# Kernel tuning notes

Measured on AMD Instinct MI355X. Metric: run time of the kernel, lower is better.

Reference implementation:

```python
import jax, jax.numpy as jnp
import numpy as np

TOPK = 20
N_SAMPLES = 100  # selects_each_sample in the torch code
SQRT2 = 1.4142   # constant used by the torch code


def _normalize(pts):
    # pts: [B,N,3] homogeneous points; weights are all-ones in the torch call path.
    c = pts.mean(axis=1)                                   # [B,3]
    d = pts - c[:, None, :]
    meandist = jnp.sqrt(d[..., 0] ** 2 + d[..., 1] ** 2).mean(axis=1)  # [B]
    s = SQRT2 / meandist
    z = jnp.zeros_like(s)
    o = jnp.ones_like(s)
    T = jnp.stack([
        jnp.stack([s, z, -c[:, 0] * s], axis=-1),
        jnp.stack([z, s, -c[:, 1] * s], axis=-1),
        jnp.stack([z, z, o], axis=-1),
    ], axis=1)                                             # [B,3,3]
    ptsn = jnp.einsum('bij,bnj->bin', T, pts)              # [B,3,N]
    return ptsn, T


def _weighted_svd(pts1, pts2, weights):
    # pts*: [B,N,3], weights: [B,1,N]. Batched (vectorized) version of the
    # per-sample torch.svd loop: smallest right-singular vector of X via eigh
    # of the 9x9 Gram matrix, then rank-2 projection of the 3x3 F via SVD.
    w = weights[:, 0, :, None]                             # [B,N,1]
    p1n, T1 = _normalize(pts1)
    p2n, T2 = _normalize(pts2)
    p = jnp.concatenate([p2n[:, 0:1] * p1n, p2n[:, 1:2] * p1n, p1n], axis=1)  # [B,9,N]
    p = jnp.swapaxes(p, 1, 2)                              # [B,N,9]
    p = p / jnp.linalg.norm(p, axis=2, keepdims=True)      # normalize_SVD=True
    X = p * w                                              # [B,N,9]
    G = jnp.einsum('bni,bnj->bij', X, X)                   # [B,9,9]
    _, evecs = jnp.linalg.eigh(G)
    v = evecs[..., 0]                                      # [B,9] min-eigvec == V[:,-1] of svd(X)
    # canonical sign (torch SVD sign is arbitrary): largest-|.| entry positive
    imax = jnp.argmax(jnp.abs(v), axis=1)
    sgn = jnp.sign(jnp.take_along_axis(v, imax[:, None], axis=1))
    v = v * sgn                                            # unit norm already
    Fm = v.reshape(-1, 3, 3)
    U, S, Vh = jnp.linalg.svd(Fm, full_matrices=False)
    S2 = S * jnp.array([1.0, 1.0, 0.0], dtype=S.dtype)     # mask = [1,1,0]
    F_ = (U * S2[:, None, :]) @ Vh                         # rank-2 projection
    out = jnp.einsum('bji,bjk,bkl->bil', T2, F_, T1)       # T2^T @ F_ @ T1
    residual = jnp.einsum('bni,bi->bn', X, v)              # [B,N]
    return out, residual


def _forward(pts1, pts2, weights, unique_nums, sampled_idx):
    B, N, _ = pts1.shape
    # 1) full weighted 8-point fit
    out, residual = _weighted_svd(pts1, pts2, weights)
    wvec = weights[:, 0, :]                                # [B,N]
    # 2) topK fit over the first `unique_num` entries (masked top_k)
    valid = jnp.arange(N)[None, :] < unique_nums[:, None]
    wm = jnp.where(valid, wvec, -jnp.inf)
    _, idx = jax.lax.top_k(wm, TOPK)                       # [B,20]
    pts1_k = jnp.take_along_axis(pts1, idx[:, :, None], axis=1)
    pts2_k = jnp.take_along_axis(pts2, idx[:, :, None], axis=1)
    w_k = jnp.take_along_axis(wvec, idx, axis=1)[:, None, :]  # [B,1,20]
    out_k, res_k = _weighted_svd(pts1_k, pts2_k, w_k)
    # 3) weighted random subsets (indices precomputed in setup_inputs)
    S_, K_ = sampled_idx.shape[1], sampled_idx.shape[2]
    bidx = jnp.arange(B)[:, None, None]
    p1s = pts1[bidx, sampled_idx]                          # [B,S,K,3]
    p2s = pts2[bidx, sampled_idx]
    ws = wvec[bidx, sampled_idx]                           # [B,S,K]
    w_accu = jnp.prod(ws * 1000.0, axis=2)                 # [B,S]
    w_accu = w_accu / (w_accu.sum(axis=1, keepdims=True) + 1e-10)
    out_s, _ = _weighted_svd(p1s.reshape(B * S_, K_, 3),
                             p2s.reshape(B * S_, K_, 3),
                             ws.reshape(B * S_, 1, K_))
    out_s = out_s.reshape(B, S_, 3, 3)
    return (out, residual, out_k, res_k, out_s, w_accu[..., None])


def setup_inputs() -> dict:
    B, N = 128, 8192
    key = jax.random.key(0)
    k1, k2, k3, k4 = jax.random.split(key, 4)
    pts1 = jax.random.normal(k1, (B, N, 3), dtype=jnp.float32).at[..., 2].set(1.0)
    pts2 = jax.random.normal(k2, (B, N, 3), dtype=jnp.float32).at[..., 2].set(1.0)
    # small positive weights so prod(w*1000, K=20) stays in fp32 range
    weights = jax.random.uniform(k3, (B, 1, N), dtype=jnp.float32) * 0.01 + 1e-6
    un = jax.random.randint(k4, (B,), 1024, N + 1).astype(jnp.int32)
    # per-sample weighted sampling (np.random.choice in the torch code)
    wnp = np.asarray(weights)[:, 0, :].astype(np.float64)
    un_np = np.asarray(un)
    rng = np.random.default_rng(0)
    sampled = np.empty((B, N_SAMPLES, TOPK), np.int32)
    for b in range(B):
        m = int(un_np[b])
        p = wnp[b, :m] / wnp[b, :m].sum()
        sampled[b] = rng.choice(m, size=(N_SAMPLES, TOPK), p=p).astype(np.int32)
    return {"pts1": pts1, "pts2": pts2, "weights": weights,
            "matches_good_unique_nums": un, "sampled_idx": jnp.asarray(sampled)}


def reference(pts1, pts2, weights, matches_good_unique_nums, sampled_idx):
    # returns (out, residual, out_topK, residual_topK,
    #          out_sample_selected_batch, weights_sample_selected_accu_batch)
    return _forward(pts1, pts2, weights, matches_good_unique_nums, sampled_idx)
```

## Files before the change

kernel.cpp:

```cpp
#include <hip/hip_runtime.h>
#include <math.h>

#define NPTS   8192
#define NB     128
#define TOPKN  20
#define NSAMP  100
#define NPROB  (NB + NB + NB * NSAMP)
#define SQRT2C 1.4142

#define OFF_OUT  0
#define OFF_RES  1152
#define OFF_OUTK 1049728
#define OFF_RESK 1050880
#define OFF_OUTS 1053440
#define OFF_WACC 1168640

#define WS_G    0
#define WS_TP   4700160
#define WS_V    5326848
#define WS_TOPK 6266880

__device__ __forceinline__ constexpr int tri9(int i, int j) {
  int a = i < j ? i : j;
  int b = i < j ? j : i;
  return a * 9 - a * (a - 1) / 2 + (b - a);
}

__global__ __launch_bounds__(1024) void prep_kernel(
    const float* __restrict__ pts1, const float* __restrict__ pts2,
    const float* __restrict__ wv, const int* __restrict__ un,
    int* __restrict__ topkidx, double* __restrict__ Gall,
    double* __restrict__ Tpall) {
  __shared__ float sw[NPTS];
  __shared__ float r16a[16], r16b[16], r16c[16], r16d[16];
  __shared__ int   i16[16];
  __shared__ double sred[16][45];
  __shared__ float sbc[6];
  const int tid = threadIdx.x, lane = tid & 63, wid = tid >> 6;

  if (blockIdx.x < NB) {
    const int b = blockIdx.x;
    const int m = un[b];
    const int mlim = (m + 1023) & ~1023;
    for (int n = tid; n < mlim; n += 1024)
      sw[n] = (n < m) ? wv[(size_t)b * NPTS + n] : -INFINITY;
    __syncthreads();
    for (int k = 0; k < TOPKN; ++k) {
      float best = -INFINITY; int bi = 0x7fffffff;
      for (int n = tid; n < mlim; n += 1024) {
        float v = sw[n];
        if (v > best) { best = v; bi = n; }
      }
      #pragma unroll
      for (int off = 32; off > 0; off >>= 1) {
        float ov = __shfl_down(best, off);
        int   oi = __shfl_down(bi, off);
        if (ov > best || (ov == best && oi < bi)) { best = ov; bi = oi; }
      }
      if (lane == 0) { r16a[wid] = best; i16[wid] = bi; }
      __syncthreads();
      if (wid == 0) {
        float v = (lane < 16) ? r16a[lane] : -INFINITY;
        int  ix = (lane < 16) ? i16[lane] : 0x7fffffff;
        #pragma unroll
        for (int off = 8; off > 0; off >>= 1) {
          float ov = __shfl_down(v, off);
          int   oi = __shfl_down(ix, off);
          if (ov > v || (ov == v && oi < ix)) { v = ov; ix = oi; }
        }
        if (lane == 0) { topkidx[b * TOPKN + k] = ix; sw[ix] = -INFINITY; }
      }
      __syncthreads();
    }
    return;
  }

  const int b = blockIdx.x - NB;
  const float* P1 = pts1 + (size_t)b * NPTS * 3;
  const float* P2 = pts2 + (size_t)b * NPTS * 3;
  const float* W  = wv   + (size_t)b * NPTS;

  float x1[8], y1[8], x2[8], y2[8], ww8[8];
  #pragma unroll
  for (int i = 0; i < 8; ++i) {
    const int n = tid + i * 1024;
    x1[i] = P1[n * 3]; y1[i] = P1[n * 3 + 1];
    x2[i] = P2[n * 3]; y2[i] = P2[n * 3 + 1];
    ww8[i] = W[n];
  }

  float sx1 = 0, sy1 = 0, sx2 = 0, sy2 = 0;
  #pragma unroll
  for (int i = 0; i < 8; ++i) { sx1 += x1[i]; sy1 += y1[i]; sx2 += x2[i]; sy2 += y2[i]; }
  #pragma unroll
  for (int off = 32; off > 0; off >>= 1) {
    sx1 += __shfl_down(sx1, off); sy1 += __shfl_down(sy1, off);
    sx2 += __shfl_down(sx2, off); sy2 += __shfl_down(sy2, off);
  }
  if (lane == 0) { r16a[wid] = sx1; r16b[wid] = sy1; r16c[wid] = sx2; r16d[wid] = sy2; }
  __syncthreads();
  if (wid == 0) {
    float a = (lane < 16) ? r16a[lane] : 0.f;
    float bb = (lane < 16) ? r16b[lane] : 0.f;
    float c = (lane < 16) ? r16c[lane] : 0.f;
    float d = (lane < 16) ? r16d[lane] : 0.f;
    #pragma unroll
    for (int off = 8; off > 0; off >>= 1) {
      a += __shfl_down(a, off); bb += __shfl_down(bb, off);
      c += __shfl_down(c, off); d += __shfl_down(d, off);
    }
    if (lane == 0) {
      sbc[0] = a / NPTS; sbc[1] = bb / NPTS; sbc[2] = c / NPTS; sbc[3] = d / NPTS;
    }
  }
  __syncthreads();
  const float cx1 = sbc[0], cy1 = sbc[1], cx2 = sbc[2], cy2 = sbc[3];

  float d1 = 0, d2 = 0;
  #pragma unroll
  for (int i = 0; i < 8; ++i) {
    float ax = x1[i] - cx1, ay = y1[i] - cy1;
    float bx = x2[i] - cx2, by = y2[i] - cy2;
    d1 += sqrtf(ax * ax + ay * ay);
    d2 += sqrtf(bx * bx + by * by);
  }
  #pragma unroll
  for (int off = 32; off > 0; off >>= 1) { d1 += __shfl_down(d1, off); d2 += __shfl_down(d2, off); }
  __syncthreads();
  if (lane == 0) { r16a[wid] = d1; r16b[wid] = d2; }
  __syncthreads();
  if (wid == 0) {
    float a = (lane < 16) ? r16a[lane] : 0.f;
    float bb = (lane < 16) ? r16b[lane] : 0.f;
    #pragma unroll
    for (int off = 8; off > 0; off >>= 1) { a += __shfl_down(a, off); bb += __shfl_down(bb, off); }
    if (lane == 0) {
      sbc[4] = (float)SQRT2C / (a / NPTS);
      sbc[5] = (float)SQRT2C / (bb / NPTS);
    }
  }
  __syncthreads();
  const float s1 = sbc[4], s2 = sbc[5];

  float g[45];
  #pragma unroll
  for (int i = 0; i < 45; ++i) g[i] = 0.f;
  #pragma unroll
  for (int i = 0; i < 8; ++i) {
    float p1x = s1 * (x1[i] - cx1), p1y = s1 * (y1[i] - cy1);
    float p2x = s2 * (x2[i] - cx2), p2y = s2 * (y2[i] - cy2);
    float f[9] = { p2x * p1x, p2x * p1y, p2x,
                   p2y * p1x, p2y * p1y, p2y,
                   p1x, p1y, 1.f };
    float n2 = 0.f;
    #pragma unroll
    for (int j = 0; j < 9; ++j) n2 += f[j] * f[j];
    float sc = ww8[i] / sqrtf(n2);
    #pragma unroll
    for (int j = 0; j < 9; ++j) f[j] *= sc;
    int t = 0;
    #pragma unroll
    for (int a = 0; a < 9; ++a)
      #pragma unroll
      for (int c = a; c < 9; ++c) { g[t] += f[a] * f[c]; ++t; }
  }
  #pragma unroll
  for (int t = 0; t < 45; ++t) {
    float v = g[t];
    #pragma unroll
    for (int off = 32; off > 0; off >>= 1) v += __shfl_down(v, off);
    if (lane == 0) sred[wid][t] = (double)v;
  }
  __syncthreads();
  if (tid < 45) {
    double a = 0;
    #pragma unroll
    for (int w = 0; w < 16; ++w) a += sred[w][tid];
    Gall[(size_t)tid * NPROB + b] = a;
  }
  if (tid == 0) {
    Tpall[0 * NPROB + b] = (double)s1;  Tpall[1 * NPROB + b] = (double)cx1;
    Tpall[2 * NPROB + b] = (double)cy1; Tpall[3 * NPROB + b] = (double)s2;
    Tpall[4 * NPROB + b] = (double)cx2; Tpall[5 * NPROB + b] = (double)cy2;
  }
}

__global__ __launch_bounds__(256) void small_g_kernel(
    const float* __restrict__ pts1, const float* __restrict__ pts2,
    const float* __restrict__ wv, const int* __restrict__ topkidx,
    const int* __restrict__ sampled, double* __restrict__ Gall,
    double* __restrict__ Tpall) {
  const int p = blockIdx.x * blockDim.x + threadIdx.x;
  if (p >= NB + NB * NSAMP) return;
  const int prob = NB + p;
  int b; const int* idx;
  if (p < NB) { b = p; idx = topkidx + p * TOPKN; }
  else { int q = p - NB; b = q / NSAMP; idx = sampled + (size_t)q * TOPKN; }
  const float* P1 = pts1 + (size_t)b * NPTS * 3;
  const float* P2 = pts2 + (size_t)b * NPTS * 3;
  const float* W  = wv   + (size_t)b * NPTS;

  float x1[TOPKN], y1[TOPKN], x2[TOPKN], y2[TOPKN], ww[TOPKN];
  #pragma unroll
  for (int k = 0; k < TOPKN; ++k) {
    int n = idx[k];
    x1[k] = P1[n * 3]; y1[k] = P1[n * 3 + 1];
    x2[k] = P2[n * 3]; y2[k] = P2[n * 3 + 1];
    ww[k] = W[n];
  }
  float cx1 = 0, cy1 = 0, cx2 = 0, cy2 = 0;
  #pragma unroll
  for (int k = 0; k < TOPKN; ++k) { cx1 += x1[k]; cy1 += y1[k]; cx2 += x2[k]; cy2 += y2[k]; }
  cx1 /= TOPKN; cy1 /= TOPKN; cx2 /= TOPKN; cy2 /= TOPKN;
  float d1 = 0, d2 = 0;
  #pragma unroll
  for (int k = 0; k < TOPKN; ++k) {
    float ax = x1[k] - cx1, ay = y1[k] - cy1; d1 += sqrtf(ax * ax + ay * ay);
    float bx = x2[k] - cx2, by = y2[k] - cy2; d2 += sqrtf(bx * bx + by * by);
  }
  const float s1 = (float)SQRT2C / (d1 / TOPKN), s2 = (float)SQRT2C / (d2 / TOPKN);

  float g[45];
  #pragma unroll
  for (int i = 0; i < 45; ++i) g[i] = 0.f;
  #pragma unroll
  for (int k = 0; k < TOPKN; ++k) {
    float p1x = s1 * (x1[k] - cx1), p1y = s1 * (y1[k] - cy1);
    float p2x = s2 * (x2[k] - cx2), p2y = s2 * (y2[k] - cy2);
    float f[9] = { p2x * p1x, p2x * p1y, p2x,
                   p2y * p1x, p2y * p1y, p2y,
                   p1x, p1y, 1.f };
    float n2 = 0.f;
    #pragma unroll
    for (int i = 0; i < 9; ++i) n2 += f[i] * f[i];
    float sc = ww[k] / sqrtf(n2);
    #pragma unroll
    for (int i = 0; i < 9; ++i) f[i] *= sc;
    int t = 0;
    #pragma unroll
    for (int i = 0; i < 9; ++i)
      #pragma unroll
      for (int j = i; j < 9; ++j) { g[t] += f[i] * f[j]; ++t; }
  }
  #pragma unroll
  for (int i = 0; i < 45; ++i) Gall[(size_t)i * NPROB + prob] = (double)g[i];
  Tpall[0 * NPROB + prob] = (double)s1;  Tpall[1 * NPROB + prob] = (double)cx1;
  Tpall[2 * NPROB + prob] = (double)cy1; Tpall[3 * NPROB + prob] = (double)s2;
  Tpall[4 * NPROB + prob] = (double)cx2; Tpall[5 * NPROB + prob] = (double)cy2;
}

__global__ __launch_bounds__(64, 1) void solve_kernel(
    const double* __restrict__ Gall, const double* __restrict__ Tpall,
    double* __restrict__ vall, float* __restrict__ dout) {
  const int prob = blockIdx.x * 64 + threadIdx.x;
  if (prob >= NPROB) return;

  float g[45];
  #pragma unroll
  for (int i = 0; i < 45; ++i) g[i] = (float)Gall[(size_t)i * NPROB + prob];

  float Vf[9][9];
  #pragma unroll
  for (int i = 0; i < 9; ++i)
    #pragma unroll
    for (int j = 0; j < 9; ++j) Vf[i][j] = (i == j) ? 1.0f : 0.0f;

  for (int sweep = 0; sweep < 5; ++sweep) {
    #pragma unroll
    for (int p = 0; p < 9; ++p) {
      #pragma unroll
      for (int q = p + 1; q < 9; ++q) {
        float apq = g[tri9(p, q)];
        if (fabsf(apq) > 1e-30f) {
          float app = g[tri9(p, p)], aqq = g[tri9(q, q)];
          float thf = (aqq - app) / (2.0f * apq);
          float tf = 1.0f / (fabsf(thf) + sqrtf(1.0f + thf * thf));
          if (thf < 0.0f) tf = -tf;
          float cf = 1.0f / sqrtf(1.0f + tf * tf);
          float sf = tf * cf;
          float tauf = sf / (1.0f + cf);
          g[tri9(p, p)] = app - tf * apq;
          g[tri9(q, q)] = aqq + tf * apq;
          g[tri9(p, q)] = 0.0f;
          #pragma unroll
          for (int k = 0; k < 9; ++k) {
            if (k != p && k != q) {
              float akp = g[tri9(k, p)], akq = g[tri9(k, q)];
              g[tri9(k, p)] = akp - sf * (akq + tauf * akp);
              g[tri9(k, q)] = akq + sf * (akp - tauf * akq);
            }
          }
          #pragma unroll
          for (int k = 0; k < 9; ++k) {
            float a = Vf[k][p], b2 = Vf[k][q];
            Vf[k][p] = cf * a - sf * b2;
            Vf[k][q] = sf * a + cf * b2;
          }
        }
      }
    }
  }

  int imin = 0; float emin = g[tri9(0, 0)];
  #pragma unroll
  for (int i = 1; i < 9; ++i) {
    float d = g[tri9(i, i)];
    if (d < emin) { emin = d; imin = i; }
  }
  double v[9];
  #pragma unroll
  for (int k = 0; k < 9; ++k) v[k] = (double)Vf[k][0];
  #pragma unroll
  for (int j = 1; j < 9; ++j) {
    bool take = (j == imin);
    #pragma unroll
    for (int k = 0; k < 9; ++k) v[k] = take ? (double)Vf[k][j] : v[k];
  }
  {
    double n2 = 0;
    #pragma unroll
    for (int i = 0; i < 9; ++i) n2 += v[i] * v[i];
    double inv = 1.0 / sqrt(n2);
    #pragma unroll
    for (int i = 0; i < 9; ++i) v[i] *= inv;
  }
  int imax = 0; double amax = fabs(v[0]);
  #pragma unroll
  for (int i = 1; i < 9; ++i) { double a = fabs(v[i]); if (a > amax) { amax = a; imax = i; } }
  double vmax = v[0];
  #pragma unroll
  for (int i = 1; i < 9; ++i) vmax = (i == imax) ? v[i] : vmax;
  double sgn = (vmax > 0.0) ? 1.0 : ((vmax < 0.0) ? -1.0 : 0.0);
  #pragma unroll
  for (int i = 0; i < 9; ++i) v[i] *= sgn;

  #pragma unroll
  for (int i = 0; i < 9; ++i) vall[(size_t)i * NPROB + prob] = v[i];

  double F[3][3] = { { v[0], v[1], v[2] }, { v[3], v[4], v[5] }, { v[6], v[7], v[8] } };
  double M[3][3];
  #pragma unroll
  for (int i = 0; i < 3; ++i)
    #pragma unroll
    for (int j = 0; j < 3; ++j) {
      double acc = 0;
      #pragma unroll
      for (int k = 0; k < 3; ++k) acc += F[k][i] * F[k][j];
      M[i][j] = acc;
    }
  double W3[3][3] = { { 1, 0, 0 }, { 0, 1, 0 }, { 0, 0, 1 } };
  for (int sweep = 0; sweep < 6; ++sweep) {
    #pragma unroll
    for (int p = 0; p < 3; ++p) {
      #pragma unroll
      for (int q = p + 1; q < 3; ++q) {
        double apq = M[p][q];
        if (fabs(apq) > 1e-30) {
          float thf = (float)(M[q][q] - M[p][p]) / (2.0f * (float)apq);
          float tf = 1.0f / (fabsf(thf) + sqrtf(1.0f + thf * thf));
          if (thf < 0.0f) tf = -tf;
          float cf = 1.0f / sqrtf(1.0f + tf * tf);
          float sf = tf * cf;
          double c = (double)cf, s = (double)sf;
          #pragma unroll
          for (int k = 0; k < 3; ++k) {
            double a = M[k][p], bq = M[k][q];
            M[k][p] = c * a - s * bq; M[k][q] = s * a + c * bq;
          }
          #pragma unroll
          for (int k = 0; k < 3; ++k) {
            double a = M[p][k], bq = M[q][k];
            M[p][k] = c * a - s * bq; M[q][k] = s * a + c * bq;
          }
          #pragma unroll
          for (int k = 0; k < 3; ++k) {
            double a = W3[k][p], bq = W3[k][q];
            W3[k][p] = c * a - s * bq; W3[k][q] = s * a + c * bq;
          }
        }
      }
    }
  }
  int i3 = 0; double e3 = M[0][0];
  if (M[1][1] < e3) { e3 = M[1][1]; i3 = 1; }
  if (M[2][2] < e3) { e3 = M[2][2]; i3 = 2; }
  double v3[3];
  #pragma unroll
  for (int k = 0; k < 3; ++k) v3[k] = W3[k][0];
  #pragma unroll
  for (int j = 1; j < 3; ++j) {
    bool take = (j == i3);
    #pragma unroll
    for (int k = 0; k < 3; ++k) v3[k] = take ? W3[k][j] : v3[k];
  }
  double Fv[3];
  #pragma unroll
  for (int i = 0; i < 3; ++i) Fv[i] = F[i][0] * v3[0] + F[i][1] * v3[1] + F[i][2] * v3[2];
  double Fr[3][3];
  #pragma unroll
  for (int i = 0; i < 3; ++i)
    #pragma unroll
    for (int j = 0; j < 3; ++j) Fr[i][j] = F[i][j] - Fv[i] * v3[j];

  double s1 = Tpall[0 * NPROB + prob], cx1 = Tpall[1 * NPROB + prob], cy1 = Tpall[2 * NPROB + prob];
  double s2 = Tpall[3 * NPROB + prob], cx2 = Tpall[4 * NPROB + prob], cy2 = Tpall[5 * NPROB + prob];
  double B1[3][3];
  #pragma unroll
  for (int i = 0; i < 3; ++i) {
    B1[i][0] = Fr[i][0] * s1;
    B1[i][1] = Fr[i][1] * s1;
    B1[i][2] = -Fr[i][0] * s1 * cx1 - Fr[i][1] * s1 * cy1 + Fr[i][2];
  }
  double O[3][3];
  #pragma unroll
  for (int l = 0; l < 3; ++l) {
    O[0][l] = s2 * B1[0][l];
    O[1][l] = s2 * B1[1][l];
    O[2][l] = -cx2 * s2 * B1[0][l] - cy2 * s2 * B1[1][l] + B1[2][l];
  }
  float* dst;
  if (prob < NB)            dst = dout + OFF_OUT  + prob * 9;
  else if (prob < 2 * NB)   dst = dout + OFF_OUTK + (prob - NB) * 9;
  else                      dst = dout + OFF_OUTS + (size_t)(prob - 2 * NB) * 9;
  #pragma unroll
  for (int i = 0; i < 3; ++i)
    #pragma unroll
    for (int j = 0; j < 3; ++j) dst[i * 3 + j] = (float)O[i][j];
}

__device__ inline double resid_point(double s1, double cx1, double cy1,
                                     double s2, double cx2, double cy2,
                                     float x1, float y1, float x2, float y2,
                                     float w, const double* __restrict__ v) {
  double p1x = s1 * ((double)x1 - cx1), p1y = s1 * ((double)y1 - cy1);
  double p2x = s2 * ((double)x2 - cx2), p2y = s2 * ((double)y2 - cy2);
  double f0 = p2x * p1x, f1 = p2x * p1y, f2 = p2x;
  double f3 = p2y * p1x, f4 = p2y * p1y, f5 = p2y;
  double f6 = p1x, f7 = p1y, f8 = 1.0;
  double n2 = f0 * f0 + f1 * f1 + f2 * f2 + f3 * f3 + f4 * f4 + f5 * f5 +
              f6 * f6 + f7 * f7 + f8 * f8;
  double sc = (double)w / sqrt(n2);
  double dt = f0 * v[0] + f1 * v[1] + f2 * v[2] + f3 * v[3] + f4 * v[4] +
              f5 * v[5] + f6 * v[6] + f7 * v[7] + f8 * v[8];
  return sc * dt;
}

__global__ __launch_bounds__(256) void tail_kernel(
    const float* __restrict__ pts1, const float* __restrict__ pts2,
    const float* __restrict__ wv, const int* __restrict__ topkidx,
    const int* __restrict__ sampled, const double* __restrict__ Tpall,
    const double* __restrict__ vall, float* __restrict__ dout) {
  const int bid = blockIdx.x, tid = threadIdx.x;
  if (bid < NB * (NPTS / 256)) {
    const int b = bid >> 5;
    const int n = (bid & 31) * 256 + tid;
    double Tp[6], v[9];
    #pragma unroll
    for (int j = 0; j < 6; ++j) Tp[j] = Tpall[(size_t)j * NPROB + b];
    #pragma unroll
    for (int j = 0; j < 9; ++j) v[j] = vall[(size_t)j * NPROB + b];
    const float* P1 = pts1 + ((size_t)b * NPTS + n) * 3;
    const float* P2 = pts2 + ((size_t)b * NPTS + n) * 3;
    float w = wv[(size_t)b * NPTS + n];
    double r = resid_point(Tp[0], Tp[1], Tp[2], Tp[3], Tp[4], Tp[5],
                           P1[0], P1[1], P2[0], P2[1], w, v);
    dout[OFF_RES + (size_t)b * NPTS + n] = (float)r;
    return;
  }
  const int b = bid - NB * (NPTS / 256);
  if (tid < TOPKN) {
    const int prob = NB + b;
    double Tp[6], v[9];
    #pragma unroll
    for (int j = 0; j < 6; ++j) Tp[j] = Tpall[(size_t)j * NPROB + prob];
    #pragma unroll
    for (int j = 0; j < 9; ++j) v[j] = vall[(size_t)j * NPROB + prob];
    int n = topkidx[b * TOPKN + tid];
    const float* P1 = pts1 + ((size_t)b * NPTS + n) * 3;
    const float* P2 = pts2 + ((size_t)b * NPTS + n) * 3;
    float w = wv[(size_t)b * NPTS + n];
    double r = resid_point(Tp[0], Tp[1], Tp[2], Tp[3], Tp[4], Tp[5],
                           P1[0], P1[1], P2[0], P2[1], w, v);
    dout[OFF_RESK + b * TOPKN + tid] = (float)r;
  }
  __shared__ double ssum[256];
  double prod = 0.0;
  if (tid < NSAMP) {
    const int* idx = sampled + ((size_t)b * NSAMP + tid) * TOPKN;
    prod = 1.0;
    #pragma unroll
    for (int k = 0; k < TOPKN; ++k)
      prod *= (double)wv[(size_t)b * NPTS + idx[k]] * 1000.0;
  }
  ssum[tid] = prod;
  __syncthreads();
  for (int off = 128; off > 0; off >>= 1) {
    if (tid < off) ssum[tid] += ssum[tid + off];
    __syncthreads();
  }
  double tot = ssum[0];
  if (tid < NSAMP) dout[OFF_WACC + b * NSAMP + tid] = (float)(prod / (tot + 1e-10));
}

extern "C" void kernel_launch(void* const* d_in, const int* in_sizes, int n_in,
                              void* d_out, int out_size, void* d_ws, size_t ws_size,
                              hipStream_t stream) {
  const float* pts1   = (const float*)d_in[0];
  const float* pts2   = (const float*)d_in[1];
  const float* wv     = (const float*)d_in[2];
  const int* un       = (const int*)d_in[3];
  const int* sampled  = (const int*)d_in[4];
  float* dout = (float*)d_out;
  char* ws = (char*)d_ws;
  double* Gall   = (double*)(ws + WS_G);
  double* Tpall  = (double*)(ws + WS_TP);
  double* vall   = (double*)(ws + WS_V);
  int*    topkix = (int*)(ws + WS_TOPK);

  prep_kernel<<<2 * NB, 1024, 0, stream>>>(pts1, pts2, wv, un, topkix, Gall, Tpall);
  small_g_kernel<<<(NB + NB * NSAMP + 255) / 256, 256, 0, stream>>>(
      pts1, pts2, wv, topkix, sampled, Gall, Tpall);
  solve_kernel<<<(NPROB + 63) / 64, 64, 0, stream>>>(Gall, Tpall, vall, dout);
  tail_kernel<<<NB * (NPTS / 256) + NB, 256, 0, stream>>>(
      pts1, pts2, wv, topkix, sampled, Tpall, vall, dout);
}
```

Before: 218.0 us.

## Split Jacobi eigen-solve across two wavefronts and run 3x3 SVD in float

```diff
diff --git a/kernel.cpp b/kernel.cpp
--- a/kernel.cpp
+++ b/kernel.cpp
@@ -249,36 +249,51 @@
   Tpall[4 * NPROB + prob] = (double)cx2; Tpall[5 * NPROB + prob] = (double)cy2;
 }
 
-__global__ __launch_bounds__(64, 1) void solve_kernel(
+__global__ __launch_bounds__(128, 1) void solve_kernel(
     const double* __restrict__ Gall, const double* __restrict__ Tpall,
     double* __restrict__ vall, float* __restrict__ dout) {
-  const int prob = blockIdx.x * 64 + threadIdx.x;
-  if (prob >= NPROB) return;
+  __shared__ float csC[64], csS[64];
+  __shared__ int   imins[64];
+  const int tid = threadIdx.x;
+  const int pid = tid & 63;
+  const int role = tid >> 6;
+  const int prob = blockIdx.x * 64 + pid;
 
   float g[45];
-  #pragma unroll
-  for (int i = 0; i < 45; ++i) g[i] = (float)Gall[(size_t)i * NPROB + prob];
-
   float Vf[9][9];
-  #pragma unroll
-  for (int i = 0; i < 9; ++i)
-    #pragma unroll
-    for (int j = 0; j < 9; ++j) Vf[i][j] = (i == j) ? 1.0f : 0.0f;
+  if (role == 0) {
+    #pragma unroll
+    for (int i = 0; i < 45; ++i) g[i] = (float)Gall[(size_t)i * NPROB + prob];
+  } else {
+    #pragma unroll
+    for (int i = 0; i < 9; ++i)
+      #pragma unroll
+      for (int j = 0; j < 9; ++j) Vf[i][j] = (i == j) ? 1.0f : 0.0f;
+  }
 
   for (int sweep = 0; sweep < 5; ++sweep) {
     #pragma unroll
     for (int p = 0; p < 9; ++p) {
       #pragma unroll
       for (int q = p + 1; q < 9; ++q) {
-        float apq = g[tri9(p, q)];
-        if (fabsf(apq) > 1e-30f) {
-          float app = g[tri9(p, p)], aqq = g[tri9(q, q)];
-          float thf = (aqq - app) / (2.0f * apq);
-          float tf = 1.0f / (fabsf(thf) + sqrtf(1.0f + thf * thf));
-          if (thf < 0.0f) tf = -tf;
-          float cf = 1.0f / sqrtf(1.0f + tf * tf);
-          float sf = tf * cf;
-          float tauf = sf / (1.0f + cf);
+        float apq = 0.f, app = 0.f, aqq = 0.f;
+        float cf = 1.f, sf = 0.f, tf = 0.f, tauf = 0.f;
+        if (role == 0) {
+          apq = g[tri9(p, q)];
+          app = g[tri9(p, p)];
+          aqq = g[tri9(q, q)];
+          if (fabsf(apq) > 1e-30f) {
+            float thf = (aqq - app) / (2.0f * apq);
+            tf = 1.0f / (fabsf(thf) + sqrtf(1.0f + thf * thf));
+            if (thf < 0.0f) tf = -tf;
+            cf = 1.0f / sqrtf(1.0f + tf * tf);
+            sf = tf * cf;
+            tauf = sf / (1.0f + cf);
+          }
+          csC[pid] = cf; csS[pid] = sf;
+        }
+        __syncthreads();
+        if (role == 0) {
           g[tri9(p, p)] = app - tf * apq;
           g[tri9(q, q)] = aqq + tf * apq;
           g[tri9(p, q)] = 0.0f;
@@ -290,23 +305,33 @@
               g[tri9(k, q)] = akq + sf * (akp - tauf * akq);
             }
           }
+        } else {
+          float c2 = csC[pid], s2 = csS[pid];
           #pragma unroll
           for (int k = 0; k < 9; ++k) {
             float a = Vf[k][p], b2 = Vf[k][q];
-            Vf[k][p] = cf * a - sf * b2;
-            Vf[k][q] = sf * a + cf * b2;
+            Vf[k][p] = c2 * a - s2 * b2;
+            Vf[k][q] = s2 * a + c2 * b2;
           }
         }
+        __syncthreads();
       }
     }
   }
 
-  int imin = 0; float emin = g[tri9(0, 0)];
-  #pragma unroll
-  for (int i = 1; i < 9; ++i) {
-    float d = g[tri9(i, i)];
-    if (d < emin) { emin = d; imin = i; }
-  }
+  if (role == 0) {
+    int imin = 0; float emin = g[tri9(0, 0)];
+    #pragma unroll
+    for (int i = 1; i < 9; ++i) {
+      float d = g[tri9(i, i)];
+      if (d < emin) { emin = d; imin = i; }
+    }
+    imins[pid] = imin;
+  }
+  __syncthreads();
+  if (role == 0) return;
+
+  const int imin = imins[pid];
   double v[9];
   #pragma unroll
   for (int k = 0; k < 9; ++k) v[k] = (double)Vf[k][0];
@@ -338,7 +363,7 @@
   for (int i = 0; i < 9; ++i) vall[(size_t)i * NPROB + prob] = v[i];
 
   double F[3][3] = { { v[0], v[1], v[2] }, { v[3], v[4], v[5] }, { v[6], v[7], v[8] } };
-  double M[3][3];
+  float M[3][3];
   #pragma unroll
   for (int i = 0; i < 3; ++i)
     #pragma unroll
@@ -346,53 +371,53 @@
       double acc = 0;
       #pragma unroll
       for (int k = 0; k < 3; ++k) acc += F[k][i] * F[k][j];
-      M[i][j] = acc;
-    }
-  double W3[3][3] = { { 1, 0, 0 }, { 0, 1, 0 }, { 0, 0, 1 } };
+      M[i][j] = (float)acc;
+    }
+  float W3[3][3] = { { 1, 0, 0 }, { 0, 1, 0 }, { 0, 0, 1 } };
   for (int sweep = 0; sweep < 6; ++sweep) {
     #pragma unroll
     for (int p = 0; p < 3; ++p) {
       #pragma unroll
       for (int q = p + 1; q < 3; ++q) {
-        double apq = M[p][q];
-        if (fabs(apq) > 1e-30) {
-          float thf = (float)(M[q][q] - M[p][p]) / (2.0f * (float)apq);
+        float apq = M[p][q];
+        if (fabsf(apq) > 1e-30f) {
+          float thf = (M[q][q] - M[p][p]) / (2.0f * apq);
           float tf = 1.0f / (fabsf(thf) + sqrtf(1.0f + thf * thf));
           if (thf < 0.0f) tf = -tf;
           float cf = 1.0f / sqrtf(1.0f + tf * tf);
           float sf = tf * cf;
-          double c = (double)cf, s = (double)sf;
           #pragma unroll
           for (int k = 0; k < 3; ++k) {
-            double a = M[k][p], bq = M[k][q];
-            M[k][p] = c * a - s * bq; M[k][q] = s * a + c * bq;
+            float a = M[k][p], bq = M[k][q];
+            M[k][p] = cf * a - sf * bq; M[k][q] = sf * a + cf * bq;
           }
           #pragma unroll
           for (int k = 0; k < 3; ++k) {
-            double a = M[p][k], bq = M[q][k];
-            M[p][k] = c * a - s * bq; M[q][k] = s * a + c * bq;
+            float a = M[p][k], bq = M[q][k];
+            M[p][k] = cf * a - sf * bq; M[q][k] = sf * a + cf * bq;
           }
           #pragma unroll
           for (int k = 0; k < 3; ++k) {
-            double a = W3[k][p], bq = W3[k][q];
-            W3[k][p] = c * a - s * bq; W3[k][q] = s * a + c * bq;
+            float a = W3[k][p], bq = W3[k][q];
+            W3[k][p] = cf * a - sf * bq; W3[k][q] = sf * a + cf * bq;
           }
         }
       }
     }
   }
-  int i3 = 0; double e3 = M[0][0];
+  int i3 = 0; float e3 = M[0][0];
   if (M[1][1] < e3) { e3 = M[1][1]; i3 = 1; }
   if (M[2][2] < e3) { e3 = M[2][2]; i3 = 2; }
-  double v3[3];
-  #pragma unroll
-  for (int k = 0; k < 3; ++k) v3[k] = W3[k][0];
+  float v3f[3];
+  #pragma unroll
+  for (int k = 0; k < 3; ++k) v3f[k] = W3[k][0];
   #pragma unroll
   for (int j = 1; j < 3; ++j) {
     bool take = (j == i3);
     #pragma unroll
-    for (int k = 0; k < 3; ++k) v3[k] = take ? W3[k][j] : v3[k];
-  }
+    for (int k = 0; k < 3; ++k) v3f[k] = take ? W3[k][j] : v3f[k];
+  }
+  double v3[3] = { (double)v3f[0], (double)v3f[1], (double)v3f[2] };
   double Fv[3];
   #pragma unroll
   for (int i = 0; i < 3; ++i) Fv[i] = F[i][0] * v3[0] + F[i][1] * v3[1] + F[i][2] * v3[2];
@@ -520,7 +545,7 @@
   prep_kernel<<<2 * NB, 1024, 0, stream>>>(pts1, pts2, wv, un, topkix, Gall, Tpall);
   small_g_kernel<<<(NB + NB * NSAMP + 255) / 256, 256, 0, stream>>>(
       pts1, pts2, wv, topkix, sampled, Gall, Tpall);
-  solve_kernel<<<(NPROB + 63) / 64, 64, 0, stream>>>(Gall, Tpall, vall, dout);
+  solve_kernel<<<NPROB / 64, 128, 0, stream>>>(Gall, Tpall, vall, dout);
   tail_kernel<<<NB * (NPTS / 256) + NB, 256, 0, stream>>>(
       pts1, pts2, wv, topkix, sampled, Tpall, vall, dout);
 }
```

Result: slower. 231.3 us (+6.1%).
